# Optimization experiments

Measured on AMD Instinct MI355X. Metric: run time of the kernel, lower is better.

Reference implementation:

```python
import jax, jax.numpy as jnp
import numpy as np

D_FEAT = 6
T = 64
HID = 128
N = 8192
EPS = 1e-5


def setup_inputs() -> dict:
    key = jax.random.key(0)
    ks = jax.random.split(key, 16)
    s = 0.08
    rn = lambda k, shape: jax.random.normal(k, shape, dtype=jnp.float32) * s
    return {
        "x": jax.random.normal(ks[0], (N, D_FEAT * T), dtype=jnp.float32),
        "w_ih0": rn(ks[1], (3 * HID, D_FEAT)),
        "w_hh0": rn(ks[2], (3 * HID, HID)),
        "b_ih0": rn(ks[3], (3 * HID,)),
        "b_hh0": rn(ks[4], (3 * HID,)),
        "w_ih1": rn(ks[5], (3 * HID, HID)),
        "w_hh1": rn(ks[6], (3 * HID, HID)),
        "b_ih1": rn(ks[7], (3 * HID,)),
        "b_hh1": rn(ks[8], (3 * HID,)),
        "bn1_g": jnp.ones((HID,), jnp.float32),
        "bn1_b": jnp.zeros((HID,), jnp.float32),
        "fc_w": rn(ks[9], (HID, HID)),
        "fc_b": rn(ks[10], (HID,)),
        "bn2_g": jnp.ones((HID,), jnp.float32),
        "bn2_b": jnp.zeros((HID,), jnp.float32),
        "fco_w": rn(ks[11], (1, HID)),
        "fco_b": rn(ks[12], (1,)),
    }


def _gru_layer(xs, w_ih, w_hh, b_ih, b_hh):
    # xs: [T, N, in] -> per-step hidden states [T, N, H] (torch nn.GRU math)
    H = w_hh.shape[1]
    gi_all = jnp.einsum('tni,gi->tng', xs, w_ih) + b_ih  # precompute input gates [T,N,3H]

    def step(h, gi):
        gh = h @ w_hh.T + b_hh
        i_r, i_z, i_n = jnp.split(gi, 3, axis=1)
        h_r, h_z, h_n = jnp.split(gh, 3, axis=1)
        r = jax.nn.sigmoid(i_r + h_r)
        z = jax.nn.sigmoid(i_z + h_z)
        n = jnp.tanh(i_n + r * h_n)
        h_new = (1.0 - z) * n + z * h
        return h_new, h_new

    h0 = jnp.zeros((xs.shape[1], H), dtype=xs.dtype)
    _, hs = jax.lax.scan(step, h0, gi_all)
    return hs


def _bn(x, g, b):
    # BatchNorm1d with track_running_stats=False: always uses batch stats
    mu = jnp.mean(x, axis=0)
    var = jnp.mean((x - mu) ** 2, axis=0)
    return (x - mu) * jax.lax.rsqrt(var + EPS) * g + b


def reference(x, w_ih0, w_hh0, b_ih0, b_hh0, w_ih1, w_hh1, b_ih1, b_hh1,
              bn1_g, bn1_b, fc_w, fc_b, bn2_g, bn2_b, fco_w, fco_b):
    n = x.shape[0]
    # reshape(N, d_feat, T).permute(0,2,1) -> time-major [T, N, d_feat] for scan
    xs = x.reshape(n, D_FEAT, T).transpose(2, 0, 1)
    h1 = _gru_layer(xs, w_ih0, w_hh0, b_ih0, b_hh0)
    h2 = _gru_layer(h1, w_ih1, w_hh1, b_ih1, b_hh1)
    hidden = _bn(h2[-1], bn1_g, bn1_b)  # [N, H]
    # cal_attention: mean_d(h_i * h_j) - mean(h_i)*mean(h_j)
    #   == (hidden @ hidden.T)/H - outer(row_means, row_means)  (exact identity)
    m = jnp.mean(hidden, axis=1)
    att = hidden @ hidden.T / jnp.float32(hidden.shape[1]) - jnp.outer(m, m)  # [N, N]
    out = att @ hidden              # [N, H]
    out = out @ fc_w.T + fc_b
    out = _bn(out, bn2_g, bn2_b)
    out = jax.nn.leaky_relu(out, 0.01)
    return (out @ fco_w.T + fco_b).squeeze(-1)  # [N]
```

## Files before the change

kernel.cpp:

```cpp
#include <hip/hip_runtime.h>

typedef unsigned short u16;
typedef short bf16x8 __attribute__((ext_vector_type(8)));
typedef float f32x4 __attribute__((ext_vector_type(4)));

#define NBATCH 8192

__device__ __forceinline__ f32x4 mfma16(bf16x8 a, bf16x8 b, f32x4 c) {
  return __builtin_amdgcn_mfma_f32_16x16x32_bf16(a, b, c, 0, 0, 0);
}
__device__ __forceinline__ u16 f2bf(float f) {
  unsigned int u = __float_as_uint(f);
  return (u16)((u + 0x7FFFu + ((u >> 16) & 1u)) >> 16);
}
__device__ __forceinline__ float sigm(float x) {
  return __builtin_amdgcn_rcpf(1.f + __builtin_amdgcn_exp2f(-1.44269504f * x));
}
__device__ __forceinline__ float tanh_(float x) {
  float t = __builtin_amdgcn_exp2f(2.88539008f * x);
  return 1.f - 2.f * __builtin_amdgcn_rcpf(t + 1.f);
}

__global__ void k_prep(const float* __restrict__ a, const float* __restrict__ b,
                       const float* __restrict__ c,
                       u16* __restrict__ oa, u16* __restrict__ ob, u16* __restrict__ oc) {
  int i = blockIdx.x * 256 + threadIdx.x;
  if (i < 49152) { oa[i] = f2bf(a[i]); ob[i] = f2bf(b[i]); oc[i] = f2bf(c[i]); }
}

#define WHH0_OFF 0
#define H0F_OFF  98304
#define H1F_OFF  115200
#define H0B_OFF  132096
#define H1B_OFF  140288
#define XT_OFF   148480
#define GRU_LDS  149504

__global__ __launch_bounds__(512, 2)
void k_gru(const float* __restrict__ x,
           const float* __restrict__ wih0, const float* __restrict__ bih0,
           const float* __restrict__ bhh0,
           const u16* __restrict__ whh0b, const u16* __restrict__ wih1b,
           const u16* __restrict__ whh1b,
           const float* __restrict__ bih1, const float* __restrict__ bhh1,
           float* __restrict__ hraw) {
  extern __shared__ char sm[];
  const int tid = threadIdx.x;
  const int wid = tid >> 6;
  const int lane = tid & 63;
  const int lq = lane >> 4;
  const int ul = lane & 15;
  const int u  = wid * 16 + ul;
  const int n0 = blockIdx.x * 32;
  const int sx = (ul & 7) << 4;

  for (int idx = tid; idx < 384 * 16; idx += 512) {
    int g = idx >> 4, cb = idx & 15;
    uint4 v = *(const uint4*)(whh0b + g * 128 + cb * 8);
    *(uint4*)(sm + WHH0_OFF + g * 256 + ((cb * 16) ^ ((g & 7) << 4))) = v;
  }
  for (int idx = tid; idx < 12544; idx += 512)
    *(float*)(sm + H0F_OFF + idx * 4) = 0.f;
  if (tid < 256) *(float*)(sm + XT_OFF + tid * 4) = 0.f;

  bf16x8 wih1f[3][4], whh1f[3][4];
#pragma unroll
  for (int i = 0; i < 3; ++i) {
    int g = (wid + 8 * i) * 16 + ul;
#pragma unroll
    for (int ki = 0; ki < 4; ++ki) {
      wih1f[i][ki] = *(const bf16x8*)(wih1b + g * 128 + ki * 32 + lq * 8);
      whh1f[i][ki] = *(const bf16x8*)(whh1b + g * 128 + ki * 32 + lq * 8);
    }
  }
  float wi0[3][6], bi0v[3], bh0v[3], bi1v[3], bh1v[3];
#pragma unroll
  for (int i = 0; i < 3; ++i) {
    int g = u + 128 * i;
#pragma unroll
    for (int d = 0; d < 6; ++d) wi0[i][d] = wih0[g * 6 + d];
    bi0v[i] = bih0[g]; bh0v[i] = bhh0[g];
    bi1v[i] = bih1[g]; bh1v[i] = bhh1[g];
  }

  const int xm = tid / 6, xd = tid - 6 * xm;
  const bool xact = tid < 192;
  const float* gx = x + (size_t)(n0 + xm) * 384 + xd * 64;
  float xv = xact ? gx[0] : 0.f;

  __syncthreads();

  float* h0f = (float*)(sm + H0F_OFF);
  float* h1f = (float*)(sm + H1F_OFF);

  for (int t = 0; t < 64; ++t) {
    if (xact) *(float*)(sm + XT_OFF + (xm * 8 + xd) * 4) = xv;

    f32x4 acc0[2][3];
#pragma unroll
    for (int mt = 0; mt < 2; ++mt)
#pragma unroll
      for (int i = 0; i < 3; ++i) acc0[mt][i] = (f32x4){0.f, 0.f, 0.f, 0.f};
#pragma unroll
    for (int ki = 0; ki < 4; ++ki) {
      int ko = ki * 64 + lq * 16;
      bf16x8 a0 = *(bf16x8*)(sm + H0B_OFF + ul * 256 + (ko ^ sx));
      bf16x8 a1 = *(bf16x8*)(sm + H0B_OFF + (16 + ul) * 256 + (ko ^ sx));
#pragma unroll
      for (int i = 0; i < 3; ++i) {
        int g = u + 128 * i;
        bf16x8 bw = *(bf16x8*)(sm + WHH0_OFF + g * 256 + (ko ^ ((g & 7) << 4)));
        acc0[0][i] = mfma16(a0, bw, acc0[0][i]);
        acc0[1][i] = mfma16(a1, bw, acc0[1][i]);
      }
    }
    __syncthreads();

#pragma unroll
    for (int mt = 0; mt < 2; ++mt) {
#pragma unroll
      for (int r = 0; r < 4; ++r) {
        int m = mt * 16 + lq * 4 + r;
        const float* xr = (const float*)(sm + XT_OFF + m * 32);
        float gi[3];
#pragma unroll
        for (int i = 0; i < 3; ++i) {
          float s = bi0v[i];
#pragma unroll
          for (int d = 0; d < 6; ++d) s += wi0[i][d] * xr[d];
          gi[i] = s;
        }
        float hr = acc0[mt][0][r] + bh0v[0];
        float hz = acc0[mt][1][r] + bh0v[1];
        float hn = acc0[mt][2][r] + bh0v[2];
        float rr = sigm(gi[0] + hr);
        float zz = sigm(gi[1] + hz);
        float nn = tanh_(gi[2] + rr * hn);
        float hold = h0f[m * 132 + u];
        float hnew = (1.f - zz) * nn + zz * hold;
        h0f[m * 132 + u] = hnew;
        *(u16*)(sm + H0B_OFF + m * 256 + ((u * 2) ^ ((m & 7) << 4))) = f2bf(hnew);
      }
    }
    __syncthreads();

    if (xact && t < 63) xv = gx[t + 1];

    f32x4 accA[2][3], accB[2][3];
#pragma unroll
    for (int mt = 0; mt < 2; ++mt)
#pragma unroll
      for (int i = 0; i < 3; ++i) {
        accA[mt][i] = (f32x4){0.f, 0.f, 0.f, 0.f};
        accB[mt][i] = (f32x4){0.f, 0.f, 0.f, 0.f};
      }
#pragma unroll
    for (int ki = 0; ki < 4; ++ki) {
      int ko = ki * 64 + lq * 16;
      bf16x8 p0 = *(bf16x8*)(sm + H0B_OFF + ul * 256 + (ko ^ sx));
      bf16x8 p1 = *(bf16x8*)(sm + H0B_OFF + (16 + ul) * 256 + (ko ^ sx));
      bf16x8 q0 = *(bf16x8*)(sm + H1B_OFF + ul * 256 + (ko ^ sx));
      bf16x8 q1 = *(bf16x8*)(sm + H1B_OFF + (16 + ul) * 256 + (ko ^ sx));
#pragma unroll
      for (int i = 0; i < 3; ++i) {
        accA[0][i] = mfma16(p0, wih1f[i][ki], accA[0][i]);
        accA[1][i] = mfma16(p1, wih1f[i][ki], accA[1][i]);
        accB[0][i] = mfma16(q0, whh1f[i][ki], accB[0][i]);
        accB[1][i] = mfma16(q1, whh1f[i][ki], accB[1][i]);
      }
    }
    __syncthreads();

#pragma unroll
    for (int mt = 0; mt < 2; ++mt) {
#pragma unroll
      for (int r = 0; r < 4; ++r) {
        int m = mt * 16 + lq * 4 + r;
        float ir = accA[mt][0][r] + bi1v[0];
        float iz = accA[mt][1][r] + bi1v[1];
        float in_ = accA[mt][2][r] + bi1v[2];
        float hr = accB[mt][0][r] + bh1v[0];
        float hz = accB[mt][1][r] + bh1v[1];
        float hn = accB[mt][2][r] + bh1v[2];
        float rr = sigm(ir + hr);
        float zz = sigm(iz + hz);
        float nn = tanh_(in_ + rr * hn);
        float hold = h1f[m * 132 + u];
        float hnew = (1.f - zz) * nn + zz * hold;
        h1f[m * 132 + u] = hnew;
        *(u16*)(sm + H1B_OFF + m * 256 + ((u * 2) ^ ((m & 7) << 4))) = f2bf(hnew);
      }
    }
    __syncthreads();
  }

  for (int idx = tid; idx < 4096; idx += 512) {
    int m = idx >> 7, f = idx & 127;
    hraw[(size_t)(n0 + m) * 128 + f] = h1f[m * 132 + f];
  }
}

__global__ void k_bn1p(const float* __restrict__ hraw, float* __restrict__ p) {
  __shared__ float s0[256], s1[256];
  int tid = threadIdx.x, b = blockIdx.x;
  int f = tid & 127, r = tid >> 7;
  float s = 0.f, q = 0.f;
  for (int n = b * 64 + r; n < b * 64 + 64; n += 2) {
    float v = hraw[(size_t)n * 128 + f];
    s += v; q += v * v;
  }
  s0[tid] = s; s1[tid] = q;
  __syncthreads();
  if (tid < 128) {
    p[b * 256 + tid] = s0[tid] + s0[tid + 128];
    p[b * 256 + 128 + tid] = s1[tid] + s1[tid + 128];
  }
}

__global__ void k_bn1r(const float* __restrict__ p, float* __restrict__ mu1,
                       float* __restrict__ rs1) {
  int f = threadIdx.x;
  float s = 0.f, q = 0.f;
  for (int b = 0; b < 128; ++b) { s += p[b * 256 + f]; q += p[b * 256 + 128 + f]; }
  float mu = s / 8192.f, var = q / 8192.f - mu * mu;
  mu1[f] = mu; rs1[f] = rsqrtf(var + 1e-5f);
}

__global__ void k_attp(const float* __restrict__ hraw, const float* __restrict__ mu1,
                       const float* __restrict__ rs1, const float* __restrict__ g1,
                       const float* __restrict__ b1, float* __restrict__ hidden,
                       float* __restrict__ mvec, float* __restrict__ gpart,
                       float* __restrict__ mhpart) {
  __shared__ float hid[64][128];
  __shared__ float mld[64];
  int tid = threadIdx.x, blk = blockIdx.x, n0 = blk * 64;
  for (int idx = tid; idx < 64 * 128; idx += 256) {
    int n = idx >> 7, f = idx & 127;
    float v = (hraw[(size_t)(n0 + n) * 128 + f] - mu1[f]) * rs1[f] * g1[f] + b1[f];
    hid[n][f] = v;
    hidden[(size_t)(n0 + n) * 128 + f] = v;
  }
  __syncthreads();
  if (tid < 64) {
    float s = 0.f;
    for (int f = 0; f < 128; ++f) s += hid[tid][f];
    s *= (1.f / 128.f);
    mld[tid] = s; mvec[n0 + tid] = s;
  }
  __syncthreads();
  int i = tid >> 1, j0 = (tid & 1) * 64;
  float acc[64];
#pragma unroll
  for (int j = 0; j < 64; ++j) acc[j] = 0.f;
  for (int n = 0; n < 64; ++n) {
    float a = hid[n][i];
#pragma unroll
    for (int j = 0; j < 64; ++j) acc[j] += a * hid[n][j0 + j];
  }
#pragma unroll
  for (int j = 0; j < 64; ++j) gpart[(size_t)blk * 16384 + i * 128 + j0 + j] = acc[j];
  if (tid < 128) {
    float s = 0.f;
    for (int n = 0; n < 64; ++n) s += mld[n] * hid[n][tid];
    mhpart[blk * 128 + tid] = s;
  }
}

__global__ void k_attfa(const float* __restrict__ gpart, const float* __restrict__ mhpart,
                        float* __restrict__ gfull, float* __restrict__ mhfull) {
  int idx = blockIdx.x * 256 + threadIdx.x;
  float s = 0.f;
  for (int b = 0; b < 128; ++b) s += gpart[(size_t)b * 16384 + idx];
  gfull[idx] = s;
  if (blockIdx.x == 0 && threadIdx.x < 128) {
    float t = 0.f;
    for (int b = 0; b < 128; ++b) t += mhpart[b * 128 + threadIdx.x];
    mhfull[threadIdx.x] = t;
  }
}

__global__ void k_attfb(const float* __restrict__ gfull, const float* __restrict__ mhfull,
                        const float* __restrict__ fcw, float* __restrict__ m2,
                        float* __restrict__ uvec) {
  int idx = blockIdx.x * 128 + threadIdx.x;
  int k = idx >> 7, j = idx & 127;
  const float4* ga = (const float4*)(gfull + k * 128);
  const float4* fb = (const float4*)(fcw + j * 128);
  float a0 = 0.f, a1 = 0.f, a2 = 0.f, a3 = 0.f;
#pragma unroll 8
  for (int f = 0; f < 32; ++f) {
    float4 a = ga[f], b = fb[f];
    a0 += a.x * b.x; a1 += a.y * b.y; a2 += a.z * b.z; a3 += a.w * b.w;
  }
  m2[idx] = (a0 + a1 + a2 + a3) * (1.f / 128.f);
  if (idx < 128) {
    float s = 0.f;
    const float* fr = fcw + idx * 128;
#pragma unroll 8
    for (int f = 0; f < 128; ++f) s += mhfull[f] * fr[f];
    uvec[idx] = s;
  }
}

__global__ void k_out2(const float* __restrict__ hidden, const float* __restrict__ mvec,
                       const float* __restrict__ m2g, const float* __restrict__ uvec,
                       const float* __restrict__ fcb, float* __restrict__ out2,
                       float* __restrict__ bn2p) {
  extern __shared__ char smo[];
  float* m2l = (float*)smo;
  float* hl = m2l + 16384;
  float* ml = hl + 4096;
  float* red = ml + 32;
  int tid = threadIdx.x, blk = blockIdx.x, n0 = blk * 32;
  for (int idx = tid; idx < 16384; idx += 256) m2l[idx] = m2g[idx];
  for (int idx = tid; idx < 4096; idx += 256) hl[idx] = hidden[(size_t)n0 * 128 + idx];
  if (tid < 32) ml[tid] = mvec[n0 + tid];
  __syncthreads();
  int j = tid & 127, rg = tid >> 7;
  float uj = uvec[j], bj = fcb[j];
  float s1 = 0.f, s2 = 0.f;
  for (int q = 0; q < 16; ++q) {
    int nl = rg * 16 + q;
    float s = bj - ml[nl] * uj;
    const float* hr = hl + nl * 128;
#pragma unroll 8
    for (int k = 0; k < 128; ++k) s += hr[k] * m2l[k * 128 + j];
    out2[(size_t)(n0 + nl) * 128 + j] = s;
    s1 += s; s2 += s * s;
  }
  red[tid] = s1; red[256 + tid] = s2;
  __syncthreads();
  if (tid < 128) {
    bn2p[blk * 256 + tid] = red[tid] + red[128 + tid];
    bn2p[blk * 256 + 128 + tid] = red[256 + tid] + red[384 + tid];
  }
}

__global__ void k_bn2(const float* __restrict__ bn2p, float* __restrict__ mu2,
                      float* __restrict__ rs2) {
  int j = threadIdx.x;
  float s = 0.f, q = 0.f;
  for (int b = 0; b < 256; ++b) {
    s += bn2p[b * 256 + j];
    q += bn2p[b * 256 + 128 + j];
  }
  float mu = s / 8192.f, var = q / 8192.f - mu * mu;
  mu2[j] = mu; rs2[j] = rsqrtf(var + 1e-5f);
}

__global__ void k_fin(const float* __restrict__ out2, const float* __restrict__ mu2,
                      const float* __restrict__ rs2, const float* __restrict__ g2,
                      const float* __restrict__ b2, const float* __restrict__ fcow,
                      const float* __restrict__ fcob, float* __restrict__ y) {
  int tid = threadIdx.x, lane = tid & 63, w = tid >> 6;
  int n = blockIdx.x * 4 + w;
  float s = 0.f;
#pragma unroll
  for (int h = 0; h < 2; ++h) {
    int j = lane + h * 64;
    float v = (out2[(size_t)n * 128 + j] - mu2[j]) * rs2[j] * g2[j] + b2[j];
    v = fmaxf(v, 0.01f * v);
    s += v * fcow[j];
  }
  for (int off = 32; off; off >>= 1) s += __shfl_down(s, off);
  if (!lane) y[n] = s + fcob[0];
}

extern "C" void kernel_launch(void* const* d_in, const int* in_sizes, int n_in,
                              void* d_out, int out_size, void* d_ws, size_t ws_size,
                              hipStream_t stream) {
  const float* x    = (const float*)d_in[0];
  const float* wih0 = (const float*)d_in[1];
  const float* whh0 = (const float*)d_in[2];
  const float* bih0 = (const float*)d_in[3];
  const float* bhh0 = (const float*)d_in[4];
  const float* wih1 = (const float*)d_in[5];
  const float* whh1 = (const float*)d_in[6];
  const float* bih1 = (const float*)d_in[7];
  const float* bhh1 = (const float*)d_in[8];
  const float* g1   = (const float*)d_in[9];
  const float* b1   = (const float*)d_in[10];
  const float* fcw  = (const float*)d_in[11];
  const float* fcb  = (const float*)d_in[12];
  const float* g2   = (const float*)d_in[13];
  const float* b2   = (const float*)d_in[14];
  const float* fcow = (const float*)d_in[15];
  const float* fcob = (const float*)d_in[16];

  char* ws = (char*)d_ws;
  u16*   whh0b  = (u16*)(ws + 0);
  u16*   wih1b  = (u16*)(ws + 98304);
  u16*   whh1b  = (u16*)(ws + 196608);
  float* hraw   = (float*)(ws + 294912);
  float* hidden = (float*)(ws + 4489216);
  float* mvec   = (float*)(ws + 8683520);
  float* mu1    = (float*)(ws + 8716288);
  float* rs1    = (float*)(ws + 8716800);
  float* gpart  = (float*)(ws + 8717312);
  float* mhpart = (float*)(ws + 17105920);
  float* m2     = (float*)(ws + 17171456);
  float* uvec   = (float*)(ws + 17236992);
  float* out2   = (float*)(ws + 17237504);
  float* bn2p   = (float*)(ws + 21431808);
  float* mu2    = (float*)(ws + 21693952);
  float* rs2    = (float*)(ws + 21694464);
  float* gfull  = (float*)(ws + 21694976);
  float* mhfull = (float*)(ws + 21760512);

  (void)hipFuncSetAttribute((const void*)k_gru,
                            hipFuncAttributeMaxDynamicSharedMemorySize, GRU_LDS);
  (void)hipFuncSetAttribute((const void*)k_out2,
                            hipFuncAttributeMaxDynamicSharedMemorySize, 84096);

  k_prep<<<192, 256, 0, stream>>>(whh0, wih1, whh1, whh0b, wih1b, whh1b);
  k_gru<<<256, 512, GRU_LDS, stream>>>(x, wih0, bih0, bhh0, whh0b, wih1b, whh1b,
                                       bih1, bhh1, hraw);
  k_bn1p<<<128, 256, 0, stream>>>(hraw, bn2p);
  k_bn1r<<<1, 128, 0, stream>>>(bn2p, mu1, rs1);
  k_attp<<<128, 256, 0, stream>>>(hraw, mu1, rs1, g1, b1, hidden, mvec, gpart, mhpart);
  k_attfa<<<64, 256, 0, stream>>>(gpart, mhpart, gfull, mhfull);
  k_attfb<<<128, 128, 0, stream>>>(gfull, mhfull, fcw, m2, uvec);
  k_out2<<<256, 256, 84096, stream>>>(hidden, mvec, m2, uvec, fcb, out2, bn2p);
  k_bn2<<<1, 128, 0, stream>>>(bn2p, mu2, rs2);
  k_fin<<<2048, 256, 0, stream>>>(out2, mu2, rs2, g2, b2, fcow, fcob, (float*)d_out);
}
```

Before: 380.4 us.

## Double-buffer GRU hidden state, fold input projection into MFMA, drop prep kernel

Restructures the GRU recurrence kernel. The bf16 hidden-state and input buffers are double-buffered, which cuts the per-step barriers from four to one. The layer-0 input projection moves from scalar FMAs into an extra MFMA using a hi/lo bf16 split of x and the weights. The fp32 hidden state now lives in registers instead of LDS, biases are pre-folded into the accumulator initial values, and the weight bf16 conversion is done inside the kernel so the separate prep kernel is gone. The risks are more register pressure and races if the single barrier does not fully order reads against writes of the shared buffers.

```diff
diff --git a/kernel.cpp b/kernel.cpp
--- a/kernel.cpp
+++ b/kernel.cpp
@@ -13,6 +13,9 @@
   unsigned int u = __float_as_uint(f);
   return (u16)((u + 0x7FFFu + ((u >> 16) & 1u)) >> 16);
 }
+__device__ __forceinline__ float bf2f(u16 h) {
+  return __uint_as_float(((unsigned int)h) << 16);
+}
 __device__ __forceinline__ float sigm(float x) {
   return __builtin_amdgcn_rcpf(1.f + __builtin_amdgcn_exp2f(-1.44269504f * x));
 }
@@ -20,28 +23,112 @@
   float t = __builtin_amdgcn_exp2f(2.88539008f * x);
   return 1.f - 2.f * __builtin_amdgcn_rcpf(t + 1.f);
 }
-
-__global__ void k_prep(const float* __restrict__ a, const float* __restrict__ b,
-                       const float* __restrict__ c,
-                       u16* __restrict__ oa, u16* __restrict__ ob, u16* __restrict__ oc) {
-  int i = blockIdx.x * 256 + threadIdx.x;
-  if (i < 49152) { oa[i] = f2bf(a[i]); ob[i] = f2bf(b[i]); oc[i] = f2bf(c[i]); }
+__device__ __forceinline__ bf16x8 pack8(const float* p) {
+  float4 a = *(const float4*)p, b = *(const float4*)(p + 4);
+  bf16x8 r;
+  r[0] = (short)f2bf(a.x); r[1] = (short)f2bf(a.y);
+  r[2] = (short)f2bf(a.z); r[3] = (short)f2bf(a.w);
+  r[4] = (short)f2bf(b.x); r[5] = (short)f2bf(b.y);
+  r[6] = (short)f2bf(b.z); r[7] = (short)f2bf(b.w);
+  return r;
 }
 
 #define WHH0_OFF 0
-#define H0F_OFF  98304
-#define H1F_OFF  115200
-#define H0B_OFF  132096
-#define H1B_OFF  140288
-#define XT_OFF   148480
-#define GRU_LDS  149504
+#define H0B_OFF  98304
+#define H1B_OFF  114688
+#define XB_OFF   131072
+#define GRU_LDS  135168
+
+#define GRU_STEP(RD, WR, T)                                                     \
+  {                                                                             \
+    if (xact && (T) < 63) {                                                     \
+      u16 xh = f2bf(xv);                                                        \
+      u16 xl = f2bf(xv - bf2f(xh));                                             \
+      char* xw = sm + XB_OFF + (WR)*2048 + xm*64 + xd*2;                        \
+      *(u16*)xw = xh; *(u16*)(xw + 16) = xl; *(u16*)(xw + 32) = xh;             \
+      if ((T) < 62) xv = gx[(T) + 2];                                           \
+    }                                                                           \
+    f32x4 rz0[2][2], hn0[2], in0[2];                                            \
+    _Pragma("unroll") for (int mt = 0; mt < 2; ++mt) {                          \
+      rz0[mt][0] = (f32x4){brz0r, brz0r, brz0r, brz0r};                         \
+      rz0[mt][1] = (f32x4){brz0z, brz0z, brz0z, brz0z};                         \
+      hn0[mt] = (f32x4){bhn0, bhn0, bhn0, bhn0};                                \
+      in0[mt] = (f32x4){bin0, bin0, bin0, bin0};                                \
+    }                                                                           \
+    _Pragma("unroll") for (int ki = 0; ki < 4; ++ki) {                          \
+      bf16x8 a0 = *(bf16x8*)(sm + H0B_OFF + (RD)*8192 + arow0 + ad[ki]);        \
+      bf16x8 a1 = *(bf16x8*)(sm + H0B_OFF + (RD)*8192 + arow1 + ad[ki]);        \
+      bf16x8 b0 = *(bf16x8*)(sm + brow0 + ad[ki]);                              \
+      bf16x8 b1 = *(bf16x8*)(sm + brow1 + ad[ki]);                              \
+      bf16x8 b2 = *(bf16x8*)(sm + brow2 + ad[ki]);                              \
+      rz0[0][0] = mfma16(a0, b0, rz0[0][0]);                                    \
+      rz0[0][1] = mfma16(a0, b1, rz0[0][1]);                                    \
+      hn0[0]    = mfma16(a0, b2, hn0[0]);                                       \
+      rz0[1][0] = mfma16(a1, b0, rz0[1][0]);                                    \
+      rz0[1][1] = mfma16(a1, b1, rz0[1][1]);                                    \
+      hn0[1]    = mfma16(a1, b2, hn0[1]);                                       \
+    }                                                                           \
+    {                                                                           \
+      bf16x8 ax0 = *(bf16x8*)(sm + XB_OFF + (RD)*2048 + xr0);                   \
+      bf16x8 ax1 = *(bf16x8*)(sm + XB_OFF + (RD)*2048 + xr1);                   \
+      rz0[0][0] = mfma16(ax0, wf0a, rz0[0][0]);                                 \
+      rz0[0][1] = mfma16(ax0, wf0b, rz0[0][1]);                                 \
+      in0[0]    = mfma16(ax0, wf0c, in0[0]);                                    \
+      rz0[1][0] = mfma16(ax1, wf0a, rz0[1][0]);                                 \
+      rz0[1][1] = mfma16(ax1, wf0b, rz0[1][1]);                                 \
+      in0[1]    = mfma16(ax1, wf0c, in0[1]);                                    \
+    }                                                                           \
+    _Pragma("unroll") for (int mt = 0; mt < 2; ++mt)                            \
+    _Pragma("unroll") for (int r = 0; r < 4; ++r) {                             \
+      int s = mt*4 + r;                                                         \
+      float rr = sigm(rz0[mt][0][r]);                                           \
+      float zz = sigm(rz0[mt][1][r]);                                           \
+      float nn = tanh_(__builtin_fmaf(rr, hn0[mt][r], in0[mt][r]));             \
+      float h = h0s[s]; h = __builtin_fmaf(zz, h - nn, nn); h0s[s] = h;         \
+      *(u16*)(sm + H0B_OFF + (WR)*8192 + st[s]) = f2bf(h);                      \
+    }                                                                           \
+    __syncthreads();                                                            \
+    f32x4 rz1[2][2], hn1[2], in1[2];                                            \
+    _Pragma("unroll") for (int mt = 0; mt < 2; ++mt) {                          \
+      rz1[mt][0] = (f32x4){brz1r, brz1r, brz1r, brz1r};                         \
+      rz1[mt][1] = (f32x4){brz1z, brz1z, brz1z, brz1z};                         \
+      hn1[mt] = (f32x4){bhn1, bhn1, bhn1, bhn1};                                \
+      in1[mt] = (f32x4){bin1, bin1, bin1, bin1};                                \
+    }                                                                           \
+    _Pragma("unroll") for (int ki = 0; ki < 4; ++ki) {                          \
+      bf16x8 p0 = *(bf16x8*)(sm + H0B_OFF + (WR)*8192 + arow0 + ad[ki]);        \
+      bf16x8 p1 = *(bf16x8*)(sm + H0B_OFF + (WR)*8192 + arow1 + ad[ki]);        \
+      bf16x8 q0 = *(bf16x8*)(sm + H1B_OFF + (RD)*8192 + arow0 + ad[ki]);        \
+      bf16x8 q1 = *(bf16x8*)(sm + H1B_OFF + (RD)*8192 + arow1 + ad[ki]);        \
+      rz1[0][0] = mfma16(p0, wih1f[0][ki], rz1[0][0]);                          \
+      rz1[0][0] = mfma16(q0, whh1f[0][ki], rz1[0][0]);                          \
+      rz1[0][1] = mfma16(p0, wih1f[1][ki], rz1[0][1]);                          \
+      rz1[0][1] = mfma16(q0, whh1f[1][ki], rz1[0][1]);                          \
+      in1[0]    = mfma16(p0, wih1f[2][ki], in1[0]);                             \
+      hn1[0]    = mfma16(q0, whh1f[2][ki], hn1[0]);                             \
+      rz1[1][0] = mfma16(p1, wih1f[0][ki], rz1[1][0]);                          \
+      rz1[1][0] = mfma16(q1, whh1f[0][ki], rz1[1][0]);                          \
+      rz1[1][1] = mfma16(p1, wih1f[1][ki], rz1[1][1]);                          \
+      rz1[1][1] = mfma16(q1, whh1f[1][ki], rz1[1][1]);                          \
+      in1[1]    = mfma16(p1, wih1f[2][ki], in1[1]);                             \
+      hn1[1]    = mfma16(q1, whh1f[2][ki], hn1[1]);                             \
+    }                                                                           \
+    _Pragma("unroll") for (int mt = 0; mt < 2; ++mt)                            \
+    _Pragma("unroll") for (int r = 0; r < 4; ++r) {                             \
+      int s = mt*4 + r;                                                         \
+      float rr = sigm(rz1[mt][0][r]);                                           \
+      float zz = sigm(rz1[mt][1][r]);                                           \
+      float nn = tanh_(__builtin_fmaf(rr, hn1[mt][r], in1[mt][r]));             \
+      float h = h1s[s]; h = __builtin_fmaf(zz, h - nn, nn); h1s[s] = h;         \
+      *(u16*)(sm + H1B_OFF + (WR)*8192 + st[s]) = f2bf(h);                      \
+    }                                                                           \
+  }
 
 __global__ __launch_bounds__(512, 2)
 void k_gru(const float* __restrict__ x,
-           const float* __restrict__ wih0, const float* __restrict__ bih0,
-           const float* __restrict__ bhh0,
-           const u16* __restrict__ whh0b, const u16* __restrict__ wih1b,
-           const u16* __restrict__ whh1b,
+           const float* __restrict__ wih0, const float* __restrict__ whh0,
+           const float* __restrict__ bih0, const float* __restrict__ bhh0,
+           const float* __restrict__ wih1, const float* __restrict__ whh1,
            const float* __restrict__ bih1, const float* __restrict__ bhh1,
            float* __restrict__ hraw) {
   extern __shared__ char sm[];
@@ -54,150 +141,103 @@
   const int n0 = blockIdx.x * 32;
   const int sx = (ul & 7) << 4;
 
-  for (int idx = tid; idx < 384 * 16; idx += 512) {
-    int g = idx >> 4, cb = idx & 15;
-    uint4 v = *(const uint4*)(whh0b + g * 128 + cb * 8);
-    *(uint4*)(sm + WHH0_OFF + g * 256 + ((cb * 16) ^ ((g & 7) << 4))) = v;
-  }
-  for (int idx = tid; idx < 12544; idx += 512)
-    *(float*)(sm + H0F_OFF + idx * 4) = 0.f;
-  if (tid < 256) *(float*)(sm + XT_OFF + tid * 4) = 0.f;
+  for (int idx = tid; idx < 9216; idx += 512)
+    *(float*)(sm + H0B_OFF + idx * 4) = 0.f;
+  for (int idx = tid; idx < 12288; idx += 512) {
+    int g = idx >> 5, c4 = (idx & 31) * 4;
+    float4 v = *(const float4*)(whh0 + g * 128 + c4);
+    unsigned int p0 = (unsigned int)f2bf(v.x) | ((unsigned int)f2bf(v.y) << 16);
+    unsigned int p1 = (unsigned int)f2bf(v.z) | ((unsigned int)f2bf(v.w) << 16);
+    unsigned int* dst = (unsigned int*)(sm + WHH0_OFF + g * 256 + ((c4 * 2) ^ ((g & 7) << 4)));
+    dst[0] = p0; dst[1] = p1;
+  }
 
   bf16x8 wih1f[3][4], whh1f[3][4];
-#pragma unroll
-  for (int i = 0; i < 3; ++i) {
-    int g = (wid + 8 * i) * 16 + ul;
-#pragma unroll
-    for (int ki = 0; ki < 4; ++ki) {
-      wih1f[i][ki] = *(const bf16x8*)(wih1b + g * 128 + ki * 32 + lq * 8);
-      whh1f[i][ki] = *(const bf16x8*)(whh1b + g * 128 + ki * 32 + lq * 8);
-    }
-  }
-  float wi0[3][6], bi0v[3], bh0v[3], bi1v[3], bh1v[3];
 #pragma unroll
   for (int i = 0; i < 3; ++i) {
     int g = u + 128 * i;
 #pragma unroll
-    for (int d = 0; d < 6; ++d) wi0[i][d] = wih0[g * 6 + d];
-    bi0v[i] = bih0[g]; bh0v[i] = bhh0[g];
-    bi1v[i] = bih1[g]; bh1v[i] = bhh1[g];
-  }
+    for (int ki = 0; ki < 4; ++ki) {
+      wih1f[i][ki] = pack8(wih1 + g * 128 + ki * 32 + lq * 8);
+      whh1f[i][ki] = pack8(whh1 + g * 128 + ki * 32 + lq * 8);
+    }
+  }
+  bf16x8 wf0a, wf0b, wf0c;
+  {
+    u16 t0[8] = {0,0,0,0,0,0,0,0}, t1[8] = {0,0,0,0,0,0,0,0}, t2[8] = {0,0,0,0,0,0,0,0};
+    u16* ts[3] = {t0, t1, t2};
+#pragma unroll
+    for (int i = 0; i < 3; ++i) {
+      int g = u + 128 * i;
+      if (lq < 2) {
+        for (int d = 0; d < 6; ++d) ts[i][d] = f2bf(wih0[g * 6 + d]);
+      } else if (lq == 2) {
+        for (int d = 0; d < 6; ++d) {
+          float w = wih0[g * 6 + d];
+          u16 h = f2bf(w);
+          ts[i][d] = f2bf(w - bf2f(h));
+        }
+      }
+    }
+    wf0a = *(bf16x8*)t0; wf0b = *(bf16x8*)t1; wf0c = *(bf16x8*)t2;
+  }
+  const float brz0r = bih0[u] + bhh0[u];
+  const float brz0z = bih0[u + 128] + bhh0[u + 128];
+  const float bin0 = bih0[u + 256], bhn0 = bhh0[u + 256];
+  const float brz1r = bih1[u] + bhh1[u];
+  const float brz1z = bih1[u + 128] + bhh1[u + 128];
+  const float bin1 = bih1[u + 256], bhn1 = bhh1[u + 256];
+
+  int ad[4];
+#pragma unroll
+  for (int ki = 0; ki < 4; ++ki) ad[ki] = (ki * 64 + lq * 16) ^ sx;
+  const int arow0 = ul * 256, arow1 = arow0 + 4096;
+  const int xr0 = ul * 64 + lq * 16, xr1 = xr0 + 1024;
+  const int brow0 = WHH0_OFF + u * 256;
+  const int brow1 = WHH0_OFF + (u + 128) * 256;
+  const int brow2 = WHH0_OFF + (u + 256) * 256;
+  int st[8];
+#pragma unroll
+  for (int mt = 0; mt < 2; ++mt)
+#pragma unroll
+    for (int r = 0; r < 4; ++r) {
+      int m = mt * 16 + lq * 4 + r;
+      st[mt * 4 + r] = m * 256 + ((u * 2) ^ ((m & 7) << 4));
+    }
+
+  float h0s[8], h1s[8];
+#pragma unroll
+  for (int s = 0; s < 8; ++s) { h0s[s] = 0.f; h1s[s] = 0.f; }
 
   const int xm = tid / 6, xd = tid - 6 * xm;
   const bool xact = tid < 192;
   const float* gx = x + (size_t)(n0 + xm) * 384 + xd * 64;
-  float xv = xact ? gx[0] : 0.f;
-
-  __syncthreads();
-
-  float* h0f = (float*)(sm + H0F_OFF);
-  float* h1f = (float*)(sm + H1F_OFF);
-
-  for (int t = 0; t < 64; ++t) {
-    if (xact) *(float*)(sm + XT_OFF + (xm * 8 + xd) * 4) = xv;
-
-    f32x4 acc0[2][3];
-#pragma unroll
-    for (int mt = 0; mt < 2; ++mt)
-#pragma unroll
-      for (int i = 0; i < 3; ++i) acc0[mt][i] = (f32x4){0.f, 0.f, 0.f, 0.f};
-#pragma unroll
-    for (int ki = 0; ki < 4; ++ki) {
-      int ko = ki * 64 + lq * 16;
-      bf16x8 a0 = *(bf16x8*)(sm + H0B_OFF + ul * 256 + (ko ^ sx));
-      bf16x8 a1 = *(bf16x8*)(sm + H0B_OFF + (16 + ul) * 256 + (ko ^ sx));
-#pragma unroll
-      for (int i = 0; i < 3; ++i) {
-        int g = u + 128 * i;
-        bf16x8 bw = *(bf16x8*)(sm + WHH0_OFF + g * 256 + (ko ^ ((g & 7) << 4)));
-        acc0[0][i] = mfma16(a0, bw, acc0[0][i]);
-        acc0[1][i] = mfma16(a1, bw, acc0[1][i]);
-      }
+
+  __syncthreads();
+
+  float xv = 0.f;
+  if (xact) {
+    float x0 = gx[0];
+    u16 h = f2bf(x0);
+    u16 l = f2bf(x0 - bf2f(h));
+    char* p = sm + XB_OFF + xm * 64 + xd * 2;
+    *(u16*)p = h; *(u16*)(p + 16) = l; *(u16*)(p + 32) = h;
+    xv = gx[1];
+  }
+  __syncthreads();
+
+  for (int t = 0; t < 64; t += 2) {
+    GRU_STEP(0, 1, t)
+    GRU_STEP(1, 0, t + 1)
+  }
+
+#pragma unroll
+  for (int mt = 0; mt < 2; ++mt)
+#pragma unroll
+    for (int r = 0; r < 4; ++r) {
+      int m = mt * 16 + lq * 4 + r;
+      hraw[(size_t)(n0 + m) * 128 + u] = h1s[mt * 4 + r];
     }
-    __syncthreads();
-
-#pragma unroll
-    for (int mt = 0; mt < 2; ++mt) {
-#pragma unroll
-      for (int r = 0; r < 4; ++r) {
-        int m = mt * 16 + lq * 4 + r;
-        const float* xr = (const float*)(sm + XT_OFF + m * 32);
-        float gi[3];
-#pragma unroll
-        for (int i = 0; i < 3; ++i) {
-          float s = bi0v[i];
-#pragma unroll
-          for (int d = 0; d < 6; ++d) s += wi0[i][d] * xr[d];
-          gi[i] = s;
-        }
-        float hr = acc0[mt][0][r] + bh0v[0];
-        float hz = acc0[mt][1][r] + bh0v[1];
-        float hn = acc0[mt][2][r] + bh0v[2];
-        float rr = sigm(gi[0] + hr);
-        float zz = sigm(gi[1] + hz);
-        float nn = tanh_(gi[2] + rr * hn);
-        float hold = h0f[m * 132 + u];
-        float hnew = (1.f - zz) * nn + zz * hold;
-        h0f[m * 132 + u] = hnew;
-        *(u16*)(sm + H0B_OFF + m * 256 + ((u * 2) ^ ((m & 7) << 4))) = f2bf(hnew);
-      }
-    }
-    __syncthreads();
-
-    if (xact && t < 63) xv = gx[t + 1];
-
-    f32x4 accA[2][3], accB[2][3];
-#pragma unroll
-    for (int mt = 0; mt < 2; ++mt)
-#pragma unroll
-      for (int i = 0; i < 3; ++i) {
-        accA[mt][i] = (f32x4){0.f, 0.f, 0.f, 0.f};
-        accB[mt][i] = (f32x4){0.f, 0.f, 0.f, 0.f};
-      }
-#pragma unroll
-    for (int ki = 0; ki < 4; ++ki) {
-      int ko = ki * 64 + lq * 16;
-      bf16x8 p0 = *(bf16x8*)(sm + H0B_OFF + ul * 256 + (ko ^ sx));
-      bf16x8 p1 = *(bf16x8*)(sm + H0B_OFF + (16 + ul) * 256 + (ko ^ sx));
-      bf16x8 q0 = *(bf16x8*)(sm + H1B_OFF + ul * 256 + (ko ^ sx));
-      bf16x8 q1 = *(bf16x8*)(sm + H1B_OFF + (16 + ul) * 256 + (ko ^ sx));
-#pragma unroll
-      for (int i = 0; i < 3; ++i) {
-        accA[0][i] = mfma16(p0, wih1f[i][ki], accA[0][i]);
-        accA[1][i] = mfma16(p1, wih1f[i][ki], accA[1][i]);
-        accB[0][i] = mfma16(q0, whh1f[i][ki], accB[0][i]);
-        accB[1][i] = mfma16(q1, whh1f[i][ki], accB[1][i]);
-      }
-    }
-    __syncthreads();
-
-#pragma unroll
-    for (int mt = 0; mt < 2; ++mt) {
-#pragma unroll
-      for (int r = 0; r < 4; ++r) {
-        int m = mt * 16 + lq * 4 + r;
-        float ir = accA[mt][0][r] + bi1v[0];
-        float iz = accA[mt][1][r] + bi1v[1];
-        float in_ = accA[mt][2][r] + bi1v[2];
-        float hr = accB[mt][0][r] + bh1v[0];
-        float hz = accB[mt][1][r] + bh1v[1];
-        float hn = accB[mt][2][r] + bh1v[2];
-        float rr = sigm(ir + hr);
-        float zz = sigm(iz + hz);
-        float nn = tanh_(in_ + rr * hn);
-        float hold = h1f[m * 132 + u];
-        float hnew = (1.f - zz) * nn + zz * hold;
-        h1f[m * 132 + u] = hnew;
-        *(u16*)(sm + H1B_OFF + m * 256 + ((u * 2) ^ ((m & 7) << 4))) = f2bf(hnew);
-      }
-    }
-    __syncthreads();
-  }
-
-  for (int idx = tid; idx < 4096; idx += 512) {
-    int m = idx >> 7, f = idx & 127;
-    hraw[(size_t)(n0 + m) * 128 + f] = h1f[m * 132 + f];
-  }
 }
 
 __global__ void k_bn1p(const float* __restrict__ hraw, float* __restrict__ p) {
@@ -388,32 +428,28 @@
   const float* fcob = (const float*)d_in[16];
 
   char* ws = (char*)d_ws;
-  u16*   whh0b  = (u16*)(ws + 0);
-  u16*   wih1b  = (u16*)(ws + 98304);
-  u16*   whh1b  = (u16*)(ws + 196608);
-  float* hraw   = (float*)(ws + 294912);
-  float* hidden = (float*)(ws + 4489216);
-  float* mvec   = (float*)(ws + 8683520);
-  float* mu1    = (float*)(ws + 8716288);
-  float* rs1    = (float*)(ws + 8716800);
-  float* gpart  = (float*)(ws + 8717312);
-  float* mhpart = (float*)(ws + 17105920);
-  float* m2     = (float*)(ws + 17171456);
-  float* uvec   = (float*)(ws + 17236992);
-  float* out2   = (float*)(ws + 17237504);
-  float* bn2p   = (float*)(ws + 21431808);
-  float* mu2    = (float*)(ws + 21693952);
-  float* rs2    = (float*)(ws + 21694464);
-  float* gfull  = (float*)(ws + 21694976);
-  float* mhfull = (float*)(ws + 21760512);
+  float* hraw   = (float*)(ws + 0);
+  float* hidden = (float*)(ws + 4194304);
+  float* mvec   = (float*)(ws + 8388608);
+  float* mu1    = (float*)(ws + 8421376);
+  float* rs1    = (float*)(ws + 8421888);
+  float* gpart  = (float*)(ws + 8422400);
+  float* mhpart = (float*)(ws + 16811008);
+  float* m2     = (float*)(ws + 16876544);
+  float* uvec   = (float*)(ws + 16942080);
+  float* out2   = (float*)(ws + 16942592);
+  float* bn2p   = (float*)(ws + 21136896);
+  float* mu2    = (float*)(ws + 21399040);
+  float* rs2    = (float*)(ws + 21399552);
+  float* gfull  = (float*)(ws + 21400064);
+  float* mhfull = (float*)(ws + 21465600);
 
   (void)hipFuncSetAttribute((const void*)k_gru,
                             hipFuncAttributeMaxDynamicSharedMemorySize, GRU_LDS);
   (void)hipFuncSetAttribute((const void*)k_out2,
                             hipFuncAttributeMaxDynamicSharedMemorySize, 84096);
 
-  k_prep<<<192, 256, 0, stream>>>(whh0, wih1, whh1, whh0b, wih1b, whh1b);
-  k_gru<<<256, 512, GRU_LDS, stream>>>(x, wih0, bih0, bhh0, whh0b, wih1b, whh1b,
+  k_gru<<<256, 512, GRU_LDS, stream>>>(x, wih0, whh0, bih0, bhh0, wih1, whh1,
                                        bih1, bhh1, hraw);
   k_bn1p<<<128, 256, 0, stream>>>(hraw, bn2p);
   k_bn1r<<<1, 128, 0, stream>>>(bn2p, mu1, rs1);
```

Result: faster. 310.4 us (-18.4%).
